# Performance work log

Hardware: AMD Instinct MI355X
Metric: run time of the kernel (lower is better)

The kernel has to match this reference:

```python
import jax, jax.numpy as jnp
import numpy as np
import math

D_MODEL = 1024
NUM_HEADS = 16
THETA = 10000.0


def _rope(x, theta):
    # x: [b, h, n, d_k], interleaved even/odd rotation as in the torch RoPE
    n, d_k = x.shape[-2], x.shape[-1]
    powers = jnp.arange(0, d_k, 2, dtype=jnp.float32) / d_k
    freqs = 1.0 / (theta ** powers)                       # [d_k/2]
    t = jnp.arange(n, dtype=jnp.float32)
    angles = jnp.outer(t, freqs)                          # [n, d_k/2]
    cos = jnp.cos(angles).astype(x.dtype)
    sin = jnp.sin(angles).astype(x.dtype)
    x_even = x[..., 0::2]
    x_odd = x[..., 1::2]
    rot_even = x_even * cos - x_odd * sin
    rot_odd = x_even * sin + x_odd * cos
    return jnp.stack([rot_even, rot_odd], axis=-1).reshape(x.shape)


def setup_inputs() -> dict:
    key = jax.random.key(0)
    ks = jax.random.split(key, 5)
    B, N, D = 2, 2048, D_MODEL
    std = math.sqrt(2.0 / (D + D))
    x = jax.random.normal(ks[0], (B, N, D), dtype=jnp.float32)
    wq = jax.random.normal(ks[1], (D, D), dtype=jnp.float32) * std
    wk = jax.random.normal(ks[2], (D, D), dtype=jnp.float32) * std
    wv = jax.random.normal(ks[3], (D, D), dtype=jnp.float32) * std
    wo = jax.random.normal(ks[4], (D, D), dtype=jnp.float32) * std
    return {"x": x, "wq": wq, "wk": wk, "wv": wv, "wo": wo}


def reference(x, wq, wk, wv, wo):
    B, N, D = x.shape
    H = NUM_HEADS
    d_k = D // H

    def split_heads(t):  # [b, n, d] -> [b, h, n, d_k]
        return t.reshape(B, N, H, d_k).transpose(0, 2, 1, 3)

    Q = split_heads(x @ wq.T)
    K = split_heads(x @ wk.T)
    V = split_heads(x @ wv.T)

    Q = _rope(Q, THETA)
    K = _rope(K, THETA)

    scale = 1.0 / math.sqrt(d_k)
    scores = jnp.einsum('bhqd,bhkd->bhqk', Q, K) * scale   # [b,h,n,n]
    causal_mask = jnp.triu(jnp.ones((N, N), dtype=bool), k=1)
    scores = jnp.where(causal_mask, -jnp.inf, scores)
    attn = jax.nn.softmax(scores, axis=-1)
    out = jnp.einsum('bhqk,bhkd->bhqd', attn, V)           # [b,h,n,d_k]
    out = out.transpose(0, 2, 1, 3).reshape(B, N, D)
    return out @ wo.T
```

## Files before the change

### kernel.cpp

```cpp
#include <hip/hip_runtime.h>
#include <math.h>

typedef _Float16 hv8 __attribute__((ext_vector_type(8)));
typedef _Float16 hv4 __attribute__((ext_vector_type(4)));
typedef _Float16 hv2 __attribute__((ext_vector_type(2)));
typedef float f32x4 __attribute__((ext_vector_type(4)));

#define LDS_AS(p) ((__attribute__((address_space(3))) void*)(p))
#define GLB_AS(p) ((const __attribute__((address_space(1))) void*)(p))

__device__ __forceinline__ float fexp2(float x) {
  float r;
  asm("v_exp_f32 %0, %1" : "=v"(r) : "v"(x));
  return r;
}

__global__ void prep_kernel(const float* __restrict__ x, const float* __restrict__ wq,
                            const float* __restrict__ wk, const float* __restrict__ wv,
                            const float* __restrict__ wo, _Float16* __restrict__ xb,
                            _Float16* __restrict__ wqkv, _Float16* __restrict__ wob,
                            float2* __restrict__ tab) {
  const int bid = blockIdx.x;
  if (bid < 256) {
    const int idx = bid * 256 + threadIdx.x;
    const int pos = idx >> 5, i = idx & 31;
    const float freq = exp2f((float)i * (-13.287712379549449f / 32.0f));
    float s, c;
    sincosf((float)pos * freq, &s, &c);
    tab[idx] = make_float2(c, s);
    return;
  }
  const int i = ((bid - 256) * 256 + threadIdx.x) * 4;
  const float* s;
  _Float16* d;
  int r;
  if (i < 4194304) {
    s = x; d = xb; r = i;
  } else {
    const int j = i - 4194304;
    const int seg = j >> 20;
    r = j & 1048575;
    s = (seg == 0) ? wq : (seg == 1) ? wk : (seg == 2) ? wv : wo;
    d = (seg < 3) ? (wqkv + (size_t)seg * 1048576) : wob;
  }
  const float4 v = *reinterpret_cast<const float4*>(s + r);
  hv4 o = {(_Float16)v.x, (_Float16)v.y, (_Float16)v.z, (_Float16)v.w};
  *reinterpret_cast<hv4*>(d + r) = o;
}

__global__ __launch_bounds__(256) void qkv_gemm_kernel(const _Float16* __restrict__ A,
                                                       const _Float16* __restrict__ B,
                                                       _Float16* __restrict__ QK,
                                                       _Float16* __restrict__ Vt,
                                                       const float2* __restrict__ tab) {
  constexpr int K = 1024;
  __shared__ __align__(16) _Float16 As[128 * 64];
  __shared__ __align__(16) _Float16 Bs[128 * 64];
  const int t = threadIdx.x;
  const int w = t >> 6, lane = t & 63;
  const int wr = w >> 1, wc = w & 1;
  const int g = lane >> 4, lr = lane & 15;
  const int mBase = blockIdx.y * 128, nBase = blockIdx.x * 128;

  f32x4 acc[4][4];
#pragma unroll
  for (int a = 0; a < 4; a++)
#pragma unroll
    for (int bb = 0; bb < 4; bb++) acc[a][bb] = {0.f, 0.f, 0.f, 0.f};

  for (int k0 = 0; k0 < K; k0 += 64) {
#pragma unroll
    for (int i = 0; i < 4; i++) {
      const int s = i * 256 + t;
      const int r = s >> 3;
      const int cs = ((s & 7) ^ (r & 7)) * 8;
      __builtin_amdgcn_global_load_lds(GLB_AS(A + (size_t)(mBase + r) * K + k0 + cs),
                                       LDS_AS(As + s * 8), 16, 0, 0);
    }
#pragma unroll
    for (int i = 0; i < 4; i++) {
      const int s = i * 256 + t;
      const int r = s >> 3;
      const int cs = ((s & 7) ^ (r & 7)) * 8;
      __builtin_amdgcn_global_load_lds(GLB_AS(B + (size_t)(nBase + r) * K + k0 + cs),
                                       LDS_AS(Bs + s * 8), 16, 0, 0);
    }
    __syncthreads();
#pragma unroll
    for (int ks = 0; ks < 2; ks++) {
      hv8 af[4], bfr[4];
#pragma unroll
      for (int mi = 0; mi < 4; mi++) {
        const int ra = wr * 64 + mi * 16 + lr;
        af[mi] = *reinterpret_cast<const hv8*>(As + ra * 64 + (((ks * 4 + g) ^ (ra & 7)) * 8));
      }
#pragma unroll
      for (int ni = 0; ni < 4; ni++) {
        const int rb = wc * 64 + ni * 16 + lr;
        bfr[ni] = *reinterpret_cast<const hv8*>(Bs + rb * 64 + (((ks * 4 + g) ^ (rb & 7)) * 8));
      }
#pragma unroll
      for (int mi = 0; mi < 4; mi++)
#pragma unroll
        for (int ni = 0; ni < 4; ni++)
          acc[mi][ni] = __builtin_amdgcn_mfma_f32_16x16x32_f16(af[mi], bfr[ni], acc[mi][ni], 0, 0, 0);
    }
    __syncthreads();
  }

  const int rowBase = mBase + wr * 64;
  const int colBase = nBase + wc * 64;
  if (nBase < 2048) {
    const float sgn = (lr & 1) ? 1.0f : -1.0f;
#pragma unroll
    for (int mi = 0; mi < 4; mi++) {
#pragma unroll
      for (int j = 0; j < 4; j++) {
        const int row = rowBase + mi * 16 + g * 4 + j;
        const int pos = row & 2047;
#pragma unroll
        for (int ni = 0; ni < 4; ni++) {
          const int col = colBase + ni * 16 + lr;
          const float2 cs2 = tab[pos * 32 + ((col & 63) >> 1)];
          const float v = acc[mi][ni][j];
          const float pv = __shfl_xor(v, 1);
          QK[(size_t)row * 2048 + col] = (_Float16)(v * cs2.x + pv * (sgn * cs2.y));
        }
      }
    }
  } else {
    const int b = rowBase >> 11;
    const int tok0 = rowBase & 2047;
#pragma unroll
    for (int ni = 0; ni < 4; ni++) {
      const int cc = colBase - 2048 + ni * 16 + lr;
      const int h = cc >> 6, d = cc & 63;
      _Float16* vp = Vt + ((size_t)(b * 16 + h) * 64 + d) * 2048 + tok0 + g * 8;
      hv8 o1, o2;
#pragma unroll
      for (int j = 0; j < 4; j++) {
        o1[j] = (_Float16)acc[0][ni][j];
        o1[4 + j] = (_Float16)acc[1][ni][j];
        o2[j] = (_Float16)acc[2][ni][j];
        o2[4 + j] = (_Float16)acc[3][ni][j];
      }
      *reinterpret_cast<hv8*>(vp) = o1;
      *reinterpret_cast<hv8*>(vp + 32) = o2;
    }
  }
}

template <int BM, typename OutT>
__global__ __launch_bounds__(256) void gemm_nt(const _Float16* __restrict__ A,
                                               const _Float16* __restrict__ B,
                                               OutT* __restrict__ C,
                                               const int M, const int N, const int K) {
  constexpr int MI = BM / 32;
  constexpr int ALOADS = BM / 32;
  __shared__ __align__(16) _Float16 As[BM * 64];
  __shared__ __align__(16) _Float16 Bs[128 * 64];
  const int t = threadIdx.x;
  const int w = t >> 6, lane = t & 63;
  const int wr = w >> 1, wc = w & 1;
  const int g = lane >> 4, lr = lane & 15;
  const int mBase = blockIdx.y * BM, nBase = blockIdx.x * 128;

  f32x4 acc[MI][4];
#pragma unroll
  for (int a = 0; a < MI; a++)
#pragma unroll
    for (int bb = 0; bb < 4; bb++) acc[a][bb] = {0.f, 0.f, 0.f, 0.f};

  for (int k0 = 0; k0 < K; k0 += 64) {
#pragma unroll
    for (int i = 0; i < ALOADS; i++) {
      const int s = i * 256 + t;
      const int r = s >> 3;
      const int cs = ((s & 7) ^ (r & 7)) * 8;
      __builtin_amdgcn_global_load_lds(GLB_AS(A + (size_t)(mBase + r) * K + k0 + cs),
                                       LDS_AS(As + s * 8), 16, 0, 0);
    }
#pragma unroll
    for (int i = 0; i < 4; i++) {
      const int s = i * 256 + t;
      const int r = s >> 3;
      const int cs = ((s & 7) ^ (r & 7)) * 8;
      __builtin_amdgcn_global_load_lds(GLB_AS(B + (size_t)(nBase + r) * K + k0 + cs),
                                       LDS_AS(Bs + s * 8), 16, 0, 0);
    }
    __syncthreads();
#pragma unroll
    for (int ks = 0; ks < 2; ks++) {
      hv8 af[MI], bfr[4];
#pragma unroll
      for (int mi = 0; mi < MI; mi++) {
        const int ra = wr * (BM / 2) + mi * 16 + lr;
        af[mi] = *reinterpret_cast<const hv8*>(As + ra * 64 + (((ks * 4 + g) ^ (ra & 7)) * 8));
      }
#pragma unroll
      for (int ni = 0; ni < 4; ni++) {
        const int rb = wc * 64 + ni * 16 + lr;
        bfr[ni] = *reinterpret_cast<const hv8*>(Bs + rb * 64 + (((ks * 4 + g) ^ (rb & 7)) * 8));
      }
#pragma unroll
      for (int mi = 0; mi < MI; mi++)
#pragma unroll
        for (int ni = 0; ni < 4; ni++)
          acc[mi][ni] = __builtin_amdgcn_mfma_f32_16x16x32_f16(af[mi], bfr[ni], acc[mi][ni], 0, 0, 0);
    }
    __syncthreads();
  }
#pragma unroll
  for (int mi = 0; mi < MI; mi++) {
#pragma unroll
    for (int j = 0; j < 4; j++) {
      const size_t row = mBase + wr * (BM / 2) + mi * 16 + g * 4 + j;
#pragma unroll
      for (int ni = 0; ni < 4; ni++) {
        const int col = nBase + wc * 64 + ni * 16 + lr;
        C[row * N + col] = (OutT)acc[mi][ni][j];
      }
    }
  }
}

__global__ __launch_bounds__(256, 4) void attn_kernel(const _Float16* __restrict__ QK,
                                                      const _Float16* __restrict__ Vt,
                                                      _Float16* __restrict__ O) {
  __shared__ __align__(16) _Float16 Ks[2][64 * 64];
  __shared__ __align__(16) _Float16 Vs[2][64 * 64];
  const int t = threadIdx.x;
  const int w = t >> 6, lane = t & 63;
  const int g = lane >> 4, lr = lane & 15;
  const int id = blockIdx.x;
  const int j = id >> 8, r = id & 255;
  const int bh = r & 31, base = r >> 5;
  const int half = j >> 1;
  const int qt = (j & 1) ? (31 - base - 8 * half) : (base + 8 * half);
  const int m0 = qt * 64;
  const int b = bh >> 4, h = bh & 15;
  const _Float16* Qp = QK + (size_t)b * 2048 * 2048 + h * 64;
  const _Float16* Kp = Qp + 1024;
  const _Float16* Vp = Vt + (size_t)bh * 64 * 2048;
  _Float16* Op = O + (size_t)b * 2048 * 1024 + h * 64;

  const int qg = m0 + w * 16 + lr;

  hv8 qf[2];
#pragma unroll
  for (int ks = 0; ks < 2; ks++) {
    qf[ks] = *reinterpret_cast<const hv8*>(Qp + (size_t)qg * 2048 + ks * 32 + g * 8);
    qf[ks] = qf[ks] * (_Float16)0.18033688f;
  }

  const hv8 onesf = {(_Float16)1.0f, (_Float16)1.0f, (_Float16)1.0f, (_Float16)1.0f,
                     (_Float16)1.0f, (_Float16)1.0f, (_Float16)1.0f, (_Float16)1.0f};

  auto STAGE = [&](int kv0, int bi) {
#pragma unroll
    for (int i = 0; i < 2; i++) {
      const int s = i * 256 + t;
      const int rr = s >> 3;
      const int cs = ((s & 7) ^ (rr & 7)) * 8;
      __builtin_amdgcn_global_load_lds(GLB_AS(Kp + (size_t)(kv0 + rr) * 2048 + cs),
                                       LDS_AS(&Ks[bi][s * 8]), 16, 0, 0);
      __builtin_amdgcn_global_load_lds(GLB_AS(Vp + (size_t)rr * 2048 + kv0 + cs),
                                       LDS_AS(&Vs[bi][s * 8]), 16, 0, 0);
    }
  };

  f32x4 oacc[4];
#pragma unroll
  for (int d = 0; d < 4; d++) oacc[d] = {0.f, 0.f, 0.f, 0.f};
  f32x4 lacc = {0.f, 0.f, 0.f, 0.f};
  float mst = -INFINITY;

  const int nt = qt + 1;
  STAGE(0, 0);
  int cur = 0;

  for (int tt = 0; tt < nt; tt++) {
    __syncthreads();
    if (tt + 1 < nt) STAGE((tt + 1) * 64, cur ^ 1);
    const int kv0 = tt * 64;
    const _Float16* Kb = Ks[cur];
    const _Float16* Vb = Vs[cur];

    f32x4 sf[4];
#pragma unroll
    for (int nf = 0; nf < 4; nf++) sf[nf] = {0.f, 0.f, 0.f, 0.f};
#pragma unroll
    for (int ks = 0; ks < 2; ks++)
#pragma unroll
      for (int nf = 0; nf < 4; nf++) {
        const hv8 kf = *reinterpret_cast<const hv8*>(
            Kb + (nf * 16 + lr) * 64 + (((ks * 4 + g) ^ (lr & 7)) * 8));
        sf[nf] = __builtin_amdgcn_mfma_f32_16x16x32_f16(kf, qf[ks], sf[nf], 0, 0, 0);
      }

    const bool diag = (tt == nt - 1);
    float p[4][4];
#pragma unroll
    for (int nf = 0; nf < 4; nf++)
#pragma unroll
      for (int jj = 0; jj < 4; jj++) {
        float xv = sf[nf][jj];
        if (diag && (kv0 + nf * 16 + g * 4 + jj > qg)) xv = -INFINITY;
        p[nf][jj] = xv;
      }
    float r4[4];
#pragma unroll
    for (int nf = 0; nf < 4; nf++)
      r4[nf] = fmaxf(fmaxf(p[nf][0], p[nf][1]), fmaxf(p[nf][2], p[nf][3]));
    const float rm = fmaxf(fmaxf(r4[0], r4[1]), fmaxf(r4[2], r4[3]));
    if (!__all(rm <= mst + 8.0f)) {
      float rw = fmaxf(rm, __shfl_xor(rm, 16));
      rw = fmaxf(rw, __shfl_xor(rw, 32));
      const float mn = fmaxf(mst, rw);
      const float corr = fexp2(mst - mn);
#pragma unroll
      for (int d = 0; d < 4; d++) oacc[d] *= corr;
      lacc *= corr;
      mst = mn;
    }
#pragma unroll
    for (int nf = 0; nf < 4; nf++)
#pragma unroll
      for (int jj = 0; jj < 4; jj++) p[nf][jj] = fexp2(p[nf][jj] - mst);

    hv8 pf[2];
#pragma unroll
    for (int ks = 0; ks < 2; ks++) {
      const auto c0 = __builtin_amdgcn_cvt_pkrtz(p[2 * ks][0], p[2 * ks][1]);
      const auto c1 = __builtin_amdgcn_cvt_pkrtz(p[2 * ks][2], p[2 * ks][3]);
      const auto c2 = __builtin_amdgcn_cvt_pkrtz(p[2 * ks + 1][0], p[2 * ks + 1][1]);
      const auto c3 = __builtin_amdgcn_cvt_pkrtz(p[2 * ks + 1][2], p[2 * ks + 1][3]);
      pf[ks][0] = (_Float16)c0[0]; pf[ks][1] = (_Float16)c0[1];
      pf[ks][2] = (_Float16)c1[0]; pf[ks][3] = (_Float16)c1[1];
      pf[ks][4] = (_Float16)c2[0]; pf[ks][5] = (_Float16)c2[1];
      pf[ks][6] = (_Float16)c3[0]; pf[ks][7] = (_Float16)c3[1];
    }

#pragma unroll
    for (int dblk = 0; dblk < 4; dblk++) {
      const int row = dblk * 16 + lr;
#pragma unroll
      for (int ks = 0; ks < 2; ks++) {
        const hv8 vtf = *reinterpret_cast<const hv8*>(
            Vb + row * 64 + (((ks * 4 + g) ^ (row & 7)) * 8));
        oacc[dblk] = __builtin_amdgcn_mfma_f32_16x16x32_f16(vtf, pf[ks], oacc[dblk], 0, 0, 0);
      }
    }
#pragma unroll
    for (int ks = 0; ks < 2; ks++)
      lacc = __builtin_amdgcn_mfma_f32_16x16x32_f16(onesf, pf[ks], lacc, 0, 0, 0);
    cur ^= 1;
  }

  const float inv = 1.0f / lacc[0];
#pragma unroll
  for (int dblk = 0; dblk < 4; dblk++) {
    hv4 o;
#pragma unroll
    for (int jj = 0; jj < 4; jj++) o[jj] = (_Float16)(oacc[dblk][jj] * inv);
    *reinterpret_cast<hv4*>(Op + (size_t)qg * 1024 + dblk * 16 + g * 4) = o;
  }
}

extern "C" void kernel_launch(void* const* d_in, const int* in_sizes, int n_in,
                              void* d_out, int out_size, void* d_ws, size_t ws_size,
                              hipStream_t stream) {
  const float* x = (const float*)d_in[0];
  const float* wq = (const float*)d_in[1];
  const float* wk = (const float*)d_in[2];
  const float* wv = (const float*)d_in[3];
  const float* wo = (const float*)d_in[4];
  float* out = (float*)d_out;
  char* ws = (char*)d_ws;
  const size_t MB = 1ull << 20;
  _Float16* xb   = (_Float16*)(ws + 0 * MB);
  _Float16* wqkv = (_Float16*)(ws + 8 * MB);
  _Float16* wob  = (_Float16*)(ws + 14 * MB);
  _Float16* QKb  = (_Float16*)(ws + 16 * MB);
  _Float16* Vtb  = (_Float16*)(ws + 32 * MB);
  float2*   rtab = (float2*)(ws + 40 * MB);
  _Float16* Ab   = (_Float16*)(ws + 0 * MB);

  prep_kernel<<<8448, 256, 0, stream>>>(x, wq, wk, wv, wo, xb, wqkv, wob, rtab);

  qkv_gemm_kernel<<<dim3(24, 32), 256, 0, stream>>>(xb, wqkv, QKb, Vtb, rtab);

  attn_kernel<<<1024, 256, 0, stream>>>(QKb, Vtb, Ab);

  gemm_nt<64, float><<<dim3(8, 64), 256, 0, stream>>>(Ab, wob, out, 4096, 1024, 1024);
}
```

Measured before the change: 113.6 us.

## Prefetch next K tile during MFMA and split RoPE into separate kernel

Both GEMM kernels now load the whole K-slice's fragments into registers, sync, and then issue the next tile's global-to-LDS loads before running the MFMAs. This lets memory traffic overlap compute using a single LDS buffer. The RoPE rotation is moved out of the QKV GEMM epilogue into a separate vectorized kernel, removing shuffles and table loads from the epilogue at the cost of an extra read/write pass over QK. Launch bounds are also set to hint occupancy.

```diff
diff --git a/kernel.cpp b/kernel.cpp
--- a/kernel.cpp
+++ b/kernel.cpp
@@ -48,11 +48,10 @@
   *reinterpret_cast<hv4*>(d + r) = o;
 }
 
-__global__ __launch_bounds__(256) void qkv_gemm_kernel(const _Float16* __restrict__ A,
-                                                       const _Float16* __restrict__ B,
-                                                       _Float16* __restrict__ QK,
-                                                       _Float16* __restrict__ Vt,
-                                                       const float2* __restrict__ tab) {
+__global__ __launch_bounds__(256, 3) void qkv_gemm_kernel(const _Float16* __restrict__ A,
+                                                          const _Float16* __restrict__ B,
+                                                          _Float16* __restrict__ QK,
+                                                          _Float16* __restrict__ Vt) {
   constexpr int K = 1024;
   __shared__ __align__(16) _Float16 As[128 * 64];
   __shared__ __align__(16) _Float16 Bs[128 * 64];
@@ -68,7 +67,7 @@
 #pragma unroll
     for (int bb = 0; bb < 4; bb++) acc[a][bb] = {0.f, 0.f, 0.f, 0.f};
 
-  for (int k0 = 0; k0 < K; k0 += 64) {
+  auto STAGE = [&](int k0) {
 #pragma unroll
     for (int i = 0; i < 4; i++) {
       const int s = i * 256 + t;
@@ -76,55 +75,51 @@
       const int cs = ((s & 7) ^ (r & 7)) * 8;
       __builtin_amdgcn_global_load_lds(GLB_AS(A + (size_t)(mBase + r) * K + k0 + cs),
                                        LDS_AS(As + s * 8), 16, 0, 0);
-    }
-#pragma unroll
-    for (int i = 0; i < 4; i++) {
-      const int s = i * 256 + t;
-      const int r = s >> 3;
-      const int cs = ((s & 7) ^ (r & 7)) * 8;
       __builtin_amdgcn_global_load_lds(GLB_AS(B + (size_t)(nBase + r) * K + k0 + cs),
                                        LDS_AS(Bs + s * 8), 16, 0, 0);
     }
+  };
+
+  STAGE(0);
+  for (int kt = 0; kt < K / 64; kt++) {
     __syncthreads();
+    hv8 af[2][4], bfr[2][4];
 #pragma unroll
     for (int ks = 0; ks < 2; ks++) {
-      hv8 af[4], bfr[4];
 #pragma unroll
       for (int mi = 0; mi < 4; mi++) {
         const int ra = wr * 64 + mi * 16 + lr;
-        af[mi] = *reinterpret_cast<const hv8*>(As + ra * 64 + (((ks * 4 + g) ^ (ra & 7)) * 8));
+        af[ks][mi] = *reinterpret_cast<const hv8*>(As + ra * 64 + (((ks * 4 + g) ^ (ra & 7)) * 8));
       }
 #pragma unroll
       for (int ni = 0; ni < 4; ni++) {
         const int rb = wc * 64 + ni * 16 + lr;
-        bfr[ni] = *reinterpret_cast<const hv8*>(Bs + rb * 64 + (((ks * 4 + g) ^ (rb & 7)) * 8));
-      }
+        bfr[ks][ni] = *reinterpret_cast<const hv8*>(Bs + rb * 64 + (((ks * 4 + g) ^ (rb & 7)) * 8));
+      }
+    }
+    __syncthreads();
+    if (kt + 1 < K / 64) STAGE((kt + 1) * 64);
+#pragma unroll
+    for (int ks = 0; ks < 2; ks++)
 #pragma unroll
       for (int mi = 0; mi < 4; mi++)
 #pragma unroll
         for (int ni = 0; ni < 4; ni++)
-          acc[mi][ni] = __builtin_amdgcn_mfma_f32_16x16x32_f16(af[mi], bfr[ni], acc[mi][ni], 0, 0, 0);
-    }
-    __syncthreads();
+          acc[mi][ni] = __builtin_amdgcn_mfma_f32_16x16x32_f16(af[ks][mi], bfr[ks][ni], acc[mi][ni], 0, 0, 0);
   }
 
   const int rowBase = mBase + wr * 64;
   const int colBase = nBase + wc * 64;
   if (nBase < 2048) {
-    const float sgn = (lr & 1) ? 1.0f : -1.0f;
 #pragma unroll
     for (int mi = 0; mi < 4; mi++) {
 #pragma unroll
       for (int j = 0; j < 4; j++) {
-        const int row = rowBase + mi * 16 + g * 4 + j;
-        const int pos = row & 2047;
+        const size_t row = rowBase + mi * 16 + g * 4 + j;
 #pragma unroll
         for (int ni = 0; ni < 4; ni++) {
           const int col = colBase + ni * 16 + lr;
-          const float2 cs2 = tab[pos * 32 + ((col & 63) >> 1)];
-          const float v = acc[mi][ni][j];
-          const float pv = __shfl_xor(v, 1);
-          QK[(size_t)row * 2048 + col] = (_Float16)(v * cs2.x + pv * (sgn * cs2.y));
+          QK[row * 2048 + col] = (_Float16)acc[mi][ni][j];
         }
       }
     }
@@ -150,11 +145,33 @@
   }
 }
 
+__global__ void rope_qk_kernel(_Float16* __restrict__ QK, const float2* __restrict__ tab) {
+  const int idx = blockIdx.x * 256 + threadIdx.x;
+  const int row = idx >> 8;
+  const int c8 = (idx & 255) * 8;
+  const int pos = row & 2047;
+  const int i0 = (c8 & 63) >> 1;
+  const size_t off = (size_t)row * 2048 + c8;
+  hv8 v = *reinterpret_cast<const hv8*>(QK + off);
+  const float2* tp = tab + pos * 32 + i0;
+  const float4 t01 = *reinterpret_cast<const float4*>(tp);
+  const float4 t23 = *reinterpret_cast<const float4*>(tp + 2);
+  const float c[4] = {t01.x, t01.z, t23.x, t23.z};
+  const float s[4] = {t01.y, t01.w, t23.y, t23.w};
+#pragma unroll
+  for (int k = 0; k < 4; k++) {
+    const float e = (float)v[2 * k], o = (float)v[2 * k + 1];
+    v[2 * k] = (_Float16)(e * c[k] - o * s[k]);
+    v[2 * k + 1] = (_Float16)(e * s[k] + o * c[k]);
+  }
+  *reinterpret_cast<hv8*>(QK + off) = v;
+}
+
 template <int BM, typename OutT>
-__global__ __launch_bounds__(256) void gemm_nt(const _Float16* __restrict__ A,
-                                               const _Float16* __restrict__ B,
-                                               OutT* __restrict__ C,
-                                               const int M, const int N, const int K) {
+__global__ __launch_bounds__(256, 2) void gemm_nt(const _Float16* __restrict__ A,
+                                                  const _Float16* __restrict__ B,
+                                                  OutT* __restrict__ C,
+                                                  const int M, const int N, const int K) {
   constexpr int MI = BM / 32;
   constexpr int ALOADS = BM / 32;
   __shared__ __align__(16) _Float16 As[BM * 64];
@@ -171,7 +188,7 @@
 #pragma unroll
     for (int bb = 0; bb < 4; bb++) acc[a][bb] = {0.f, 0.f, 0.f, 0.f};
 
-  for (int k0 = 0; k0 < K; k0 += 64) {
+  auto STAGE = [&](int k0) {
 #pragma unroll
     for (int i = 0; i < ALOADS; i++) {
       const int s = i * 256 + t;
@@ -188,27 +205,35 @@
       __builtin_amdgcn_global_load_lds(GLB_AS(B + (size_t)(nBase + r) * K + k0 + cs),
                                        LDS_AS(Bs + s * 8), 16, 0, 0);
     }
+  };
+
+  STAGE(0);
+  const int NT = K / 64;
+  for (int kt = 0; kt < NT; kt++) {
     __syncthreads();
+    hv8 af[2][MI], bfr[2][4];
 #pragma unroll
     for (int ks = 0; ks < 2; ks++) {
-      hv8 af[MI], bfr[4];
 #pragma unroll
       for (int mi = 0; mi < MI; mi++) {
         const int ra = wr * (BM / 2) + mi * 16 + lr;
-        af[mi] = *reinterpret_cast<const hv8*>(As + ra * 64 + (((ks * 4 + g) ^ (ra & 7)) * 8));
+        af[ks][mi] = *reinterpret_cast<const hv8*>(As + ra * 64 + (((ks * 4 + g) ^ (ra & 7)) * 8));
       }
 #pragma unroll
       for (int ni = 0; ni < 4; ni++) {
         const int rb = wc * 64 + ni * 16 + lr;
-        bfr[ni] = *reinterpret_cast<const hv8*>(Bs + rb * 64 + (((ks * 4 + g) ^ (rb & 7)) * 8));
-      }
+        bfr[ks][ni] = *reinterpret_cast<const hv8*>(Bs + rb * 64 + (((ks * 4 + g) ^ (rb & 7)) * 8));
+      }
+    }
+    __syncthreads();
+    if (kt + 1 < NT) STAGE((kt + 1) * 64);
+#pragma unroll
+    for (int ks = 0; ks < 2; ks++)
 #pragma unroll
       for (int mi = 0; mi < MI; mi++)
 #pragma unroll
         for (int ni = 0; ni < 4; ni++)
-          acc[mi][ni] = __builtin_amdgcn_mfma_f32_16x16x32_f16(af[mi], bfr[ni], acc[mi][ni], 0, 0, 0);
-    }
-    __syncthreads();
+          acc[mi][ni] = __builtin_amdgcn_mfma_f32_16x16x32_f16(af[ks][mi], bfr[ks][ni], acc[mi][ni], 0, 0, 0);
   }
 #pragma unroll
   for (int mi = 0; mi < MI; mi++) {
@@ -388,7 +413,9 @@
 
   prep_kernel<<<8448, 256, 0, stream>>>(x, wq, wk, wv, wo, xb, wqkv, wob, rtab);
 
-  qkv_gemm_kernel<<<dim3(24, 32), 256, 0, stream>>>(xb, wqkv, QKb, Vtb, rtab);
+  qkv_gemm_kernel<<<dim3(24, 32), 256, 0, stream>>>(xb, wqkv, QKb, Vtb);
+
+  rope_qk_kernel<<<4096, 256, 0, stream>>>(QKb, rtab);
 
   attn_kernel<<<1024, 256, 0, stream>>>(QKb, Vtb, Ab);
 
```

After: 104.6 us. 1.09x faster.
